# Kernel tuning notes

Hardware: AMD Instinct MI355X
Metric: run time of the kernel (lower is better)

The kernel has to match this reference:

```python
import jax, jax.numpy as jnp
import numpy as np

B, S, D = 32, 512, 1024
DROPNUM = 128


def setup_inputs() -> dict:
    key = jax.random.key(0)
    k1, k2, k3, k4 = jax.random.split(key, 4)
    return {
        "in_seq": jax.random.normal(k1, (B, S, D), dtype=jnp.float32),
        "out_seq": jax.random.normal(k2, (B, S, D), dtype=jnp.float32),
        "drop_idx": jax.random.randint(k3, (B, DROPNUM), 0, S, dtype=jnp.int64),
        "keep_idx": jax.random.randint(k4, (B, S - DROPNUM), 0, S, dtype=jnp.int64),
    }


def reference(in_seq, out_seq, drop_idx, keep_idx):
    b, s, d = in_seq.shape
    dropnum = drop_idx.shape[1]

    # Batched gathers (replaces the per-batch index_select loop)
    predictions = jnp.take_along_axis(out_seq, drop_idx[:, :, None], axis=1)      # (B, dropnum, D)
    inputs = jnp.take_along_axis(in_seq, keep_idx[:, :, None], axis=1)            # (B, S-dropnum, D)
    reconstructions = jnp.take_along_axis(out_seq, keep_idx[:, :, None], axis=1)  # (B, S-dropnum, D)

    # target[i, j] = i*S + drop_idx[i, j]
    target = (jnp.arange(b, dtype=drop_idx.dtype)[:, None] * s + drop_idx).reshape(-1)  # (B*dropnum,)

    outputs = predictions.reshape(b * dropnum, d)
    keys = in_seq.reshape(b * s, d)
    # torch: outputs @ in_seq.permute(2,0,1).reshape(D, B*S)  ==  outputs @ keys.T
    lossmat = jnp.einsum("nd,md->nm", outputs, keys)  # (B*dropnum, B*S)

    # Accuracy (no-grad diagnostic in original)
    top1 = jnp.argmax(lossmat, axis=1)
    acc = jnp.mean((top1 == target).astype(jnp.float32)) * 100.0

    # Cross entropy (mean reduction, as nn.CrossEntropyLoss default)
    logp = jax.nn.log_softmax(lossmat, axis=1)
    xe = -jnp.mean(logp[jnp.arange(b * dropnum), target])

    # MSE (mean reduction)
    mse = jnp.mean((inputs - reconstructions) ** 2)

    loss = xe + mse
    return (loss, xe, mse, acc)
```

## Files before the change

### kernel.cpp

```cpp
#include <hip/hip_runtime.h>
#include <hip/hip_bf16.h>


typedef __attribute__((ext_vector_type(8))) _Float16 half8;
typedef __attribute__((ext_vector_type(4))) _Float16 half4v;
typedef __attribute__((ext_vector_type(4))) float f32x4;

#define MFMA16(a, b, c) __builtin_amdgcn_mfma_f32_16x16x32_f16((a), (b), (c), 0, 0, 0)

__device__ __forceinline__ float fexp2(float x) {
    float r;
    asm("v_exp_f32 %0, %1" : "=v"(r) : "v"(x));
    return r;
}
__device__ __forceinline__ float flog2(float x) {
    float r;
    asm("v_log_f32 %0, %1" : "=v"(r) : "v"(x));
    return r;
}

__device__ __forceinline__ void glds16(const _Float16* g, _Float16* l) {
    __builtin_amdgcn_global_load_lds(
        (const __attribute__((address_space(1))) unsigned int*)g,
        (__attribute__((address_space(3))) unsigned int*)l, 16, 0, 0);
}

__global__ void conv_k(const float* __restrict__ in_seq, const float* __restrict__ out_seq,
                       const int* __restrict__ drop, _Float16* __restrict__ Kf,
                       _Float16* __restrict__ Pf, int* __restrict__ tgt) {
    const float C = 1.4426950408889634f;
    unsigned bid = blockIdx.x;
    if (bid < 16384u) {
        unsigned t = bid * 256u + threadIdx.x;
        unsigned idx = t * 4u;
        unsigned row = idx >> 10;
        unsigned k = idx & 1023u;
        float4 v = *(const float4*)(in_seq + idx);
        unsigned d = (row << 10) + (k ^ ((row & 7u) << 3));
        half4v o = {(_Float16)v.x, (_Float16)v.y, (_Float16)v.z, (_Float16)v.w};
        *(half4v*)(Kf + d) = o;
    } else {
        unsigned t = (bid - 16384u) * 256u + threadIdx.x;
        unsigned idx = t * 4u;
        unsigned prow = idx >> 10;
        unsigned k = idx & 1023u;
        unsigned b = prow >> 7, j = prow & 127u;
        int srow = drop[b * 128u + j];
        size_t gsrc = ((size_t)((b << 9) + (unsigned)srow) << 10) + k;
        float4 v = *(const float4*)(out_seq + gsrc);
        unsigned d = (prow << 10) + (k ^ ((prow & 7u) << 3));
        half4v o = {(_Float16)(v.x * C), (_Float16)(v.y * C), (_Float16)(v.z * C),
                    (_Float16)(v.w * C)};
        *(half4v*)(Pf + d) = o;
        if (k == 0) tgt[prow] = (int)((b << 9) + (unsigned)srow);
    }
}

#define LDSB 24576

__global__ __launch_bounds__(512, 2) void gemm_stats_k(
    const _Float16* __restrict__ Pf, const _Float16* __restrict__ Kf,
    const int* __restrict__ tgt,
    float* __restrict__ pmax, float* __restrict__ psum, int* __restrict__ pidx,
    float* __restrict__ xt) {
    extern __shared__ _Float16 lds[];

    const int tid = threadIdx.x;
    const int lane = tid & 63;
    const int wave = tid >> 6;
    const int wm = wave >> 2, wn = wave & 3;
    const int lr = lane & 15, lk = lane >> 4;

    unsigned id = blockIdx.x;
    unsigned wg = (id & 7u) * 256u + (id >> 3);
    const int bn = wg & 63, bm = wg >> 6;

    const int sr = tid >> 3;
    const int sgc = tid & 7;
    const _Float16* gA = Pf + (size_t)(bm * 128 + sr) * 1024 + sgc * 8;
    const _Float16* gB = Kf + (size_t)(bn * 256 + sr) * 1024 + sgc * 8;

    f32x4 acc[4][4] = {};

    auto STAGE = [&](int buf, int kt) {
        const unsigned kof = kt * 64u;
        const unsigned base = buf * LDSB;
#pragma unroll
        for (int is = 0; is < 2; ++is)
            glds16(gA + (size_t)is * 64 * 1024 + kof, &lds[base + (is * 512 + tid) * 8]);
#pragma unroll
        for (int is = 0; is < 4; ++is)
            glds16(gB + (size_t)is * 64 * 1024 + kof, &lds[base + 8192 + (is * 512 + tid) * 8]);
    };

    auto COMPUTE = [&](int buf) {
        const _Float16* La = &lds[buf * LDSB];
        const _Float16* Lb = &lds[buf * LDSB + 8192];
#pragma unroll
        for (int ks = 0; ks < 2; ++ks) {
            half8 a[4], b[4];
#pragma unroll
            for (int i = 0; i < 4; ++i) {
                int r = wm * 64 + i * 16 + lr;
                int kl = (ks * 32 + lk * 8) ^ ((r & 7) << 3);
                a[i] = *(const half8*)&La[r * 64 + kl];
            }
#pragma unroll
            for (int n = 0; n < 4; ++n) {
                int r = wn * 64 + n * 16 + lr;
                int kl = (ks * 32 + lk * 8) ^ ((r & 7) << 3);
                b[n] = *(const half8*)&Lb[r * 64 + kl];
            }
            __builtin_amdgcn_s_setprio(1);
#pragma unroll
            for (int i = 0; i < 4; ++i)
#pragma unroll
                for (int n = 0; n < 4; ++n) acc[i][n] = MFMA16(a[i], b[n], acc[i][n]);
            __builtin_amdgcn_s_setprio(0);
        }
    };

    STAGE(0, 0);
    STAGE(1, 1);
    asm volatile("s_waitcnt vmcnt(6)" ::: "memory");
    __builtin_amdgcn_s_barrier();
    __builtin_amdgcn_sched_barrier(0);

#pragma unroll
    for (int kt = 0; kt < 16; ++kt) {
        if (kt + 2 < 16) STAGE((kt + 2) % 3, kt + 2);
        COMPUTE(kt % 3);
        if (kt < 14) {
            asm volatile("s_waitcnt vmcnt(6)" ::: "memory");
        } else if (kt == 14) {
            asm volatile("s_waitcnt vmcnt(0)" ::: "memory");
        }
        if (kt < 15) {
            __builtin_amdgcn_s_barrier();
            __builtin_amdgcn_sched_barrier(0);
        }
    }

    const int chunk = bn * 4 + wn;
#pragma unroll
    for (int i = 0; i < 4; ++i) {
#pragma unroll
        for (int j = 0; j < 4; ++j) {
            int grow = bm * 128 + wm * 64 + i * 16 + lk * 4 + j;
            int tcol = tgt[grow];
            float v0 = acc[i][0][j], v1 = acc[i][1][j], v2 = acc[i][2][j], v3 = acc[i][3][j];
            int c0 = bn * 256 + wn * 64 + lr;
            if (c0 == tcol) xt[grow] = v0;
            if (c0 + 16 == tcol) xt[grow] = v1;
            if (c0 + 32 == tcol) xt[grow] = v2;
            if (c0 + 48 == tcol) xt[grow] = v3;
            float mx = fmaxf(fmaxf(v0, v1), fmaxf(v2, v3));
#pragma unroll
            for (int off = 1; off < 16; off <<= 1) mx = fmaxf(mx, __shfl_xor(mx, off));
            int am = v0 == mx ? c0
                   : v1 == mx ? c0 + 16
                   : v2 == mx ? c0 + 32
                   : v3 == mx ? c0 + 48
                              : 0x7fffffff;
#pragma unroll
            for (int off = 1; off < 16; off <<= 1) {
                int o = __shfl_xor(am, off);
                am = o < am ? o : am;
            }
            float s = fexp2(v0 - mx) + fexp2(v1 - mx) + fexp2(v2 - mx) + fexp2(v3 - mx);
#pragma unroll
            for (int off = 1; off < 16; off <<= 1) s += __shfl_xor(s, off);
            if (lr == 0) {
                pmax[grow * 256 + chunk] = mx;
                psum[grow * 256 + chunk] = s;
                pidx[grow * 256 + chunk] = am;
            }
        }
    }
}

__global__ void pass2_k(const float* __restrict__ pmax, const float* __restrict__ psum,
                        const int* __restrict__ pidx, const float* __restrict__ xt,
                        const int* __restrict__ tgt, float* __restrict__ rxe,
                        float* __restrict__ rhit) {
    int row = blockIdx.x;
    int t = threadIdx.x;
    float m = -3.0e38f, l = 0.f;
    int ai = 0x7fffffff;
    for (int c = t; c < 256; c += 64) {
        float cm = pmax[row * 256 + c];
        float cl = psum[row * 256 + c];
        int ci = pidx[row * 256 + c];
        if (cm > m || (cm == m && ci < ai)) {
            l = l * fexp2(m - cm) + cl;
            ai = ci;
            m = cm;
        } else {
            l += cl * fexp2(cm - m);
        }
    }
#pragma unroll
    for (int off = 1; off < 64; off <<= 1) {
        float om = __shfl_xor(m, off);
        float ol = __shfl_xor(l, off);
        int oi = __shfl_xor(ai, off);
        if (om > m || (om == m && oi < ai)) {
            l = l * fexp2(m - om) + ol;
            ai = oi;
            m = om;
        } else {
            l += ol * fexp2(om - m);
        }
    }
    if (t == 0) {
        rxe[row] = (m + flog2(l) - xt[row]) * 0.69314718055994531f;
        rhit[row] = (ai == tgt[row]) ? 1.f : 0.f;
    }
}

__global__ void mse_partial_k(const float* __restrict__ inseq, const float* __restrict__ outseq,
                              const int* __restrict__ keep, float* __restrict__ msep) {
    float s = 0.f;
    for (unsigned f = blockIdx.x * 256u + threadIdx.x; f < 3145728u; f += 1024u * 256u) {
        unsigned rowid = f >> 8;
        unsigned kf = (f & 255u) << 2;
        unsigned b = rowid / 384u;
        unsigned j = rowid - b * 384u;
        int r = keep[b * 384u + j];
        size_t base = (((size_t)(b * 512u + (unsigned)r)) << 10) + kf;
        float4 a = *(const float4*)(inseq + base);
        float4 c = *(const float4*)(outseq + base);
        float dx = a.x - c.x, dy = a.y - c.y, dz = a.z - c.z, dw = a.w - c.w;
        s += dx * dx + dy * dy + dz * dz + dw * dw;
    }
#pragma unroll
    for (int off = 1; off < 64; off <<= 1) s += __shfl_xor(s, off);
    __shared__ float red[4];
    if ((threadIdx.x & 63) == 0) red[threadIdx.x >> 6] = s;
    __syncthreads();
    if (threadIdx.x == 0) msep[blockIdx.x] = red[0] + red[1] + red[2] + red[3];
}

__global__ void finalize_k(const float* __restrict__ rxe, const float* __restrict__ rhit,
                           const float* __restrict__ msep, float* __restrict__ out) {
    int tid = threadIdx.x;
    float sx = 0.f, sh = 0.f, sm = 0.f;
    for (int i = tid; i < 4096; i += 256) {
        sx += rxe[i];
        sh += rhit[i];
    }
    for (int i = tid; i < 1024; i += 256) sm += msep[i];
#pragma unroll
    for (int off = 1; off < 64; off <<= 1) {
        sx += __shfl_xor(sx, off);
        sh += __shfl_xor(sh, off);
        sm += __shfl_xor(sm, off);
    }
    __shared__ float red[3][4];
    int w = tid >> 6;
    if ((tid & 63) == 0) {
        red[0][w] = sx;
        red[1][w] = sh;
        red[2][w] = sm;
    }
    __syncthreads();
    if (tid == 0) {
        sx = red[0][0] + red[0][1] + red[0][2] + red[0][3];
        sh = red[1][0] + red[1][1] + red[1][2] + red[1][3];
        sm = red[2][0] + red[2][1] + red[2][2] + red[2][3];
        float xe = sx * (1.f / 4096.f);
        float mse = sm / (12288.f * 1024.f);
        float accp = 100.f * sh * (1.f / 4096.f);
        out[0] = xe + mse;
        out[1] = xe;
        out[2] = mse;
        out[3] = accp;
    }
}

extern "C" void kernel_launch(void* const* d_in, const int* in_sizes, int n_in,
                              void* d_out, int out_size, void* d_ws, size_t ws_size,
                              hipStream_t stream) {
    const float* in_seq = (const float*)d_in[0];
    const float* out_seq = (const float*)d_in[1];
    const int* drop = (const int*)d_in[2];
    const int* keep = (const int*)d_in[3];
    float* out = (float*)d_out;

    char* w = (char*)d_ws;
    _Float16* Kf = (_Float16*)w; w += 33554432;
    _Float16* Pf = (_Float16*)w; w += 8388608;
    float* pmax = (float*)w; w += 4194304;
    float* psum = (float*)w; w += 4194304;
    int* pidx = (int*)w; w += 4194304;
    float* xt = (float*)w; w += 16384;
    int* tgt = (int*)w; w += 16384;
    float* rxe = (float*)w; w += 16384;
    float* rhit = (float*)w; w += 16384;
    float* msep = (float*)w; w += 4096;

    (void)hipFuncSetAttribute((const void*)gemm_stats_k,
                              hipFuncAttributeMaxDynamicSharedMemorySize, 3 * LDSB * 2);

    conv_k<<<20480, 256, 0, stream>>>(in_seq, out_seq, drop, Kf, Pf, tgt);
    gemm_stats_k<<<2048, 512, 3 * LDSB * 2, stream>>>(Pf, Kf, tgt, pmax, psum, pidx, xt);
    pass2_k<<<4096, 64, 0, stream>>>(pmax, psum, pidx, xt, tgt, rxe, rhit);
    mse_partial_k<<<1024, 256, 0, stream>>>(in_seq, out_seq, keep, msep);
    finalize_k<<<1, 256, 0, stream>>>(rxe, rhit, msep, out);
}
```

Measured before the change: 379.1 us.

## Enlarge GEMM tile to 256x256 with a four-slot half-K LDS pipeline

```diff
diff --git a/kernel.cpp b/kernel.cpp
--- a/kernel.cpp
+++ b/kernel.cpp
@@ -36,7 +36,7 @@
         unsigned row = idx >> 10;
         unsigned k = idx & 1023u;
         float4 v = *(const float4*)(in_seq + idx);
-        unsigned d = (row << 10) + (k ^ ((row & 7u) << 3));
+        unsigned d = (row << 10) + (k ^ (((row >> 1) & 3u) << 3));
         half4v o = {(_Float16)v.x, (_Float16)v.y, (_Float16)v.z, (_Float16)v.w};
         *(half4v*)(Kf + d) = o;
     } else {
@@ -48,15 +48,13 @@
         int srow = drop[b * 128u + j];
         size_t gsrc = ((size_t)((b << 9) + (unsigned)srow) << 10) + k;
         float4 v = *(const float4*)(out_seq + gsrc);
-        unsigned d = (prow << 10) + (k ^ ((prow & 7u) << 3));
+        unsigned d = (prow << 10) + (k ^ (((prow >> 1) & 3u) << 3));
         half4v o = {(_Float16)(v.x * C), (_Float16)(v.y * C), (_Float16)(v.z * C),
                     (_Float16)(v.w * C)};
         *(half4v*)(Pf + d) = o;
         if (k == 0) tgt[prow] = (int)((b << 9) + (unsigned)srow);
     }
 }
-
-#define LDSB 24576
 
 __global__ __launch_bounds__(512, 2) void gemm_stats_k(
     const _Float16* __restrict__ Pf, const _Float16* __restrict__ Kf,
@@ -72,103 +70,117 @@
     const int lr = lane & 15, lk = lane >> 4;
 
     unsigned id = blockIdx.x;
-    unsigned wg = (id & 7u) * 256u + (id >> 3);
-    const int bn = wg & 63, bm = wg >> 6;
-
-    const int sr = tid >> 3;
-    const int sgc = tid & 7;
-    const _Float16* gA = Pf + (size_t)(bm * 128 + sr) * 1024 + sgc * 8;
-    const _Float16* gB = Kf + (size_t)(bn * 256 + sr) * 1024 + sgc * 8;
-
-    f32x4 acc[4][4] = {};
-
-    auto STAGE = [&](int buf, int kt) {
-        const unsigned kof = kt * 64u;
-        const unsigned base = buf * LDSB;
-#pragma unroll
-        for (int is = 0; is < 2; ++is)
-            glds16(gA + (size_t)is * 64 * 1024 + kof, &lds[base + (is * 512 + tid) * 8]);
-#pragma unroll
-        for (int is = 0; is < 4; ++is)
-            glds16(gB + (size_t)is * 64 * 1024 + kof, &lds[base + 8192 + (is * 512 + tid) * 8]);
+    unsigned wg = (id & 7u) * 128u + (id >> 3);
+    const int bn = wg >> 4, bm = wg & 15;
+
+    const _Float16* aSrc = Pf + (size_t)(bm * 256 + (tid >> 2)) * 1024 + (tid & 3) * 8;
+    const _Float16* bSrc = Kf + (size_t)(bn * 256 + (tid >> 2)) * 1024 + (tid & 3) * 8;
+
+    const unsigned swz = (unsigned)((lk ^ ((lr >> 1) & 3)) << 3);
+
+    f32x4 acc[8][4] = {};
+    half8 bfr[4];
+
+    auto STAGEP = [&](int h, int ph) {
+        const int skt = h >> 1, sks = h & 1;
+        const unsigned ss = (unsigned)(h & 3) * 16384u;
+        const unsigned go = (unsigned)(skt * 64 + sks * 32);
+        if (ph == 0) {
+            glds16(aSrc + go, &lds[ss + tid * 8]);
+            glds16(aSrc + 131072 + go, &lds[ss + 4096 + tid * 8]);
+        } else {
+            glds16(bSrc + go, &lds[ss + 8192 + tid * 8]);
+            glds16(bSrc + 131072 + go, &lds[ss + 12288 + tid * 8]);
+        }
     };
 
-    auto COMPUTE = [&](int buf) {
-        const _Float16* La = &lds[buf * LDSB];
-        const _Float16* Lb = &lds[buf * LDSB + 8192];
-#pragma unroll
-        for (int ks = 0; ks < 2; ++ks) {
-            half8 a[4], b[4];
-#pragma unroll
-            for (int i = 0; i < 4; ++i) {
-                int r = wm * 64 + i * 16 + lr;
-                int kl = (ks * 32 + lk * 8) ^ ((r & 7) << 3);
-                a[i] = *(const half8*)&La[r * 64 + kl];
-            }
-#pragma unroll
+    #pragma unroll
+    for (int h = 0; h < 4; ++h) {
+        STAGEP(h, 0);
+        STAGEP(h, 1);
+    }
+    asm volatile("s_waitcnt vmcnt(12)" ::: "memory");
+    __builtin_amdgcn_s_barrier();
+    __builtin_amdgcn_sched_barrier(0);
+
+    #pragma unroll
+    for (int p = 0; p < 64; ++p) {
+        const int q = p & 3;
+        const int ks = q >> 1, mh = q & 1;
+        const int kt = p >> 2;
+        const unsigned sb = (unsigned)((2 * kt + ks) & 3) * 16384u;
+
+        half8 a[4];
+        #pragma unroll
+        for (int i = 0; i < 4; ++i) {
+            int r = wm * 128 + mh * 64 + i * 16 + lr;
+            a[i] = *(const half8*)&lds[sb + r * 32 + swz];
+        }
+        if (q == 0 || q == 2) {
+            #pragma unroll
             for (int n = 0; n < 4; ++n) {
                 int r = wn * 64 + n * 16 + lr;
-                int kl = (ks * 32 + lk * 8) ^ ((r & 7) << 3);
-                b[n] = *(const half8*)&Lb[r * 64 + kl];
+                bfr[n] = *(const half8*)&lds[sb + 8192 + r * 32 + swz];
             }
-            __builtin_amdgcn_s_setprio(1);
-#pragma unroll
-            for (int i = 0; i < 4; ++i)
-#pragma unroll
-                for (int n = 0; n < 4; ++n) acc[i][n] = MFMA16(a[i], b[n], acc[i][n]);
-            __builtin_amdgcn_s_setprio(0);
-        }
-    };
-
-    STAGE(0, 0);
-    STAGE(1, 1);
-    asm volatile("s_waitcnt vmcnt(6)" ::: "memory");
-    __builtin_amdgcn_s_barrier();
-    __builtin_amdgcn_sched_barrier(0);
-
-#pragma unroll
-    for (int kt = 0; kt < 16; ++kt) {
-        if (kt + 2 < 16) STAGE((kt + 2) % 3, kt + 2);
-        COMPUTE(kt % 3);
-        if (kt < 14) {
-            asm volatile("s_waitcnt vmcnt(6)" ::: "memory");
-        } else if (kt == 14) {
-            asm volatile("s_waitcnt vmcnt(0)" ::: "memory");
-        }
-        if (kt < 15) {
+        }
+        if (p >= 2 && p <= 57) STAGEP(4 + (p - 2) / 2, (p - 2) & 1);
+
+        __builtin_amdgcn_s_barrier();
+        asm volatile("s_waitcnt lgkmcnt(0)" ::: "memory");
+        __builtin_amdgcn_sched_barrier(0);
+
+        __builtin_amdgcn_s_setprio(1);
+        #pragma unroll
+        for (int i = 0; i < 4; ++i)
+            #pragma unroll
+            for (int n = 0; n < 4; ++n)
+                acc[mh * 4 + i][n] = MFMA16(a[i], bfr[n], acc[mh * 4 + i][n]);
+        __builtin_amdgcn_s_setprio(0);
+
+        if (p & 1) {
+            if (p < 59) {
+                asm volatile("s_waitcnt vmcnt(8)" ::: "memory");
+            } else if (p == 59) {
+                asm volatile("s_waitcnt vmcnt(4)" ::: "memory");
+            } else if (p == 61) {
+                asm volatile("s_waitcnt vmcnt(0)" ::: "memory");
+            }
+        }
+        if (p < 63) {
             __builtin_amdgcn_s_barrier();
             __builtin_amdgcn_sched_barrier(0);
         }
     }
 
     const int chunk = bn * 4 + wn;
-#pragma unroll
-    for (int i = 0; i < 4; ++i) {
-#pragma unroll
+    #pragma unroll
+    for (int mi = 0; mi < 8; ++mi) {
+        #pragma unroll
         for (int j = 0; j < 4; ++j) {
-            int grow = bm * 128 + wm * 64 + i * 16 + lk * 4 + j;
+            int grow = bm * 256 + wm * 128 + mi * 16 + lk * 4 + j;
             int tcol = tgt[grow];
-            float v0 = acc[i][0][j], v1 = acc[i][1][j], v2 = acc[i][2][j], v3 = acc[i][3][j];
+            float v0 = acc[mi][0][j], v1 = acc[mi][1][j], v2 = acc[mi][2][j],
+                  v3 = acc[mi][3][j];
             int c0 = bn * 256 + wn * 64 + lr;
             if (c0 == tcol) xt[grow] = v0;
             if (c0 + 16 == tcol) xt[grow] = v1;
             if (c0 + 32 == tcol) xt[grow] = v2;
             if (c0 + 48 == tcol) xt[grow] = v3;
             float mx = fmaxf(fmaxf(v0, v1), fmaxf(v2, v3));
-#pragma unroll
+            #pragma unroll
             for (int off = 1; off < 16; off <<= 1) mx = fmaxf(mx, __shfl_xor(mx, off));
             int am = v0 == mx ? c0
                    : v1 == mx ? c0 + 16
                    : v2 == mx ? c0 + 32
                    : v3 == mx ? c0 + 48
                               : 0x7fffffff;
-#pragma unroll
+            #pragma unroll
             for (int off = 1; off < 16; off <<= 1) {
                 int o = __shfl_xor(am, off);
                 am = o < am ? o : am;
             }
             float s = fexp2(v0 - mx) + fexp2(v1 - mx) + fexp2(v2 - mx) + fexp2(v3 - mx);
-#pragma unroll
+            #pragma unroll
             for (int off = 1; off < 16; off <<= 1) s += __shfl_xor(s, off);
             if (lr == 0) {
                 pmax[grow * 256 + chunk] = mx;
@@ -199,7 +211,7 @@
             l += cl * fexp2(cm - m);
         }
     }
-#pragma unroll
+    #pragma unroll
     for (int off = 1; off < 64; off <<= 1) {
         float om = __shfl_xor(m, off);
         float ol = __shfl_xor(l, off);
@@ -233,7 +245,7 @@
         float dx = a.x - c.x, dy = a.y - c.y, dz = a.z - c.z, dw = a.w - c.w;
         s += dx * dx + dy * dy + dz * dz + dw * dw;
     }
-#pragma unroll
+    #pragma unroll
     for (int off = 1; off < 64; off <<= 1) s += __shfl_xor(s, off);
     __shared__ float red[4];
     if ((threadIdx.x & 63) == 0) red[threadIdx.x >> 6] = s;
@@ -250,7 +262,7 @@
         sh += rhit[i];
     }
     for (int i = tid; i < 1024; i += 256) sm += msep[i];
-#pragma unroll
+    #pragma unroll
     for (int off = 1; off < 64; off <<= 1) {
         sx += __shfl_xor(sx, off);
         sh += __shfl_xor(sh, off);
@@ -299,11 +311,15 @@
     float* rhit = (float*)w; w += 16384;
     float* msep = (float*)w; w += 4096;
 
-    (void)hipFuncSetAttribute((const void*)gemm_stats_k,
-                              hipFuncAttributeMaxDynamicSharedMemorySize, 3 * LDSB * 2);
+    static int attr_done = 0;
+    if (!attr_done) {
+        (void)hipFuncSetAttribute((const void*)gemm_stats_k,
+                                  hipFuncAttributeMaxDynamicSharedMemorySize, 131072);
+        attr_done = 1;
+    }
 
     conv_k<<<20480, 256, 0, stream>>>(in_seq, out_seq, drop, Kf, Pf, tgt);
-    gemm_stats_k<<<2048, 512, 3 * LDSB * 2, stream>>>(Pf, Kf, tgt, pmax, psum, pidx, xt);
+    gemm_stats_k<<<1024, 512, 131072, stream>>>(Pf, Kf, tgt, pmax, psum, pidx, xt);
     pass2_k<<<4096, 64, 0, stream>>>(pmax, psum, pidx, xt, tgt, rxe, rhit);
     mse_partial_k<<<1024, 256, 0, stream>>>(in_seq, out_seq, keep, msep);
     finalize_k<<<1, 256, 0, stream>>>(rxe, rhit, msep, out);
```

Result: faster. 354.6 us (-6.5%).
